# Performance work log

Hardware: AMD Instinct MI355X
Metric: run time of the kernel (lower is better)

Reference implementation:

```python
import jax, jax.numpy as jnp
import numpy as np

B, S, H = 2, 2048, 2048
NH, NKV, HD = 16, 4, 128
LAT = H // 8  # compression_ratio=8


def _rope_tables():
    inv_freq = 1.0 / (10000.0 ** (jnp.arange(0, HD, 2, dtype=jnp.float32) / HD))
    pos = jnp.arange(S, dtype=jnp.float32)
    freqs = pos[:, None] * inv_freq[None, :]          # [S, HD/2]
    emb = jnp.concatenate([freqs, freqs], axis=-1)    # [S, HD]
    return jnp.cos(emb)[None, None], jnp.sin(emb)[None, None]  # [1,1,S,HD]


def setup_inputs() -> dict:
    key = jax.random.key(0)
    ks = jax.random.split(key, 8)
    std = 0.02
    hidden_states = jax.random.normal(ks[0], (B, S, H), dtype=jnp.float32)
    cos, sin = _rope_tables()
    # additive causal mask, broadcast over batch/heads
    causal = jnp.tril(jnp.ones((S, S), dtype=bool))
    attention_mask = jnp.where(causal, 0.0, -1e9).astype(jnp.float32)[None, None]
    Wq = jax.random.normal(ks[1], (H, H), dtype=jnp.float32) * std
    Wk = jax.random.normal(ks[2], (NKV * HD, H), dtype=jnp.float32) * std
    Wv = jax.random.normal(ks[3], (NKV * HD, H), dtype=jnp.float32) * std
    Wo = jax.random.normal(ks[4], (H, H), dtype=jnp.float32) * std
    Wl_in = jax.random.normal(ks[5], (LAT, H), dtype=jnp.float32) * std
    Wl_out = jax.random.normal(ks[6], (H, LAT), dtype=jnp.float32) * std
    latent_gate = jnp.ones((1,), dtype=jnp.float32)
    return dict(hidden_states=hidden_states, cos=cos, sin=sin,
                attention_mask=attention_mask, Wq=Wq, Wk=Wk, Wv=Wv, Wo=Wo,
                Wl_in=Wl_in, Wl_out=Wl_out, latent_gate=latent_gate)


def _rotate_half(x):
    x1, x2 = jnp.split(x, 2, axis=-1)
    return jnp.concatenate([-x2, x1], axis=-1)


def reference(hidden_states, cos, sin, attention_mask, Wq, Wk, Wv, Wo,
              Wl_in, Wl_out, latent_gate):
    b, s, h = hidden_states.shape
    # projections (torch Linear: x @ W.T)
    q = (hidden_states @ Wq.T).reshape(b, s, NH, HD).transpose(0, 2, 1, 3)    # [b,nh,s,hd]
    k = (hidden_states @ Wk.T).reshape(b, s, NKV, HD).transpose(0, 2, 1, 3)   # [b,nkv,s,hd]
    v = (hidden_states @ Wv.T).reshape(b, s, NKV, HD).transpose(0, 2, 1, 3)
    # inline RoPE
    c, sn = cos[:, :, :s, :], sin[:, :, :s, :]
    q = q * c + _rotate_half(q) * sn
    k = k * c + _rotate_half(k) * sn
    # GQA: replicate kv heads (repeat_interleave along head dim)
    rep = NH // NKV
    k = jnp.repeat(k, rep, axis=1)
    v = jnp.repeat(v, rep, axis=1)
    scores = jnp.einsum('bhqd,bhkd->bhqk', q, k) / np.sqrt(HD).astype(np.float32)
    scores = scores + attention_mask
    attn = jax.nn.softmax(scores, axis=-1)
    ctx = jnp.einsum('bhqk,bhkd->bhqd', attn, v)          # [b,nh,s,hd]
    ctx = ctx.transpose(0, 2, 1, 3).reshape(b, s, h)
    attn_out = ctx @ Wo.T
    latent = (hidden_states @ Wl_in.T) @ Wl_out.T          # low-rank residual branch
    return attn_out + latent_gate * latent
```

## Files before the change

### kernel.cpp

```cpp
#include <hip/hip_runtime.h>
#include <hip/hip_bf16.h>

#define Bn   2
#define Sn   2048
#define Hn   2048
#define NHn  16
#define NKVn 4
#define HDn  128
#define LATn 256
#define Mn   (Bn*Sn)
#define KC   2304
#define NWn  3328

typedef unsigned short ushort_t;
typedef __attribute__((ext_vector_type(8))) short bf16x8;
typedef __attribute__((ext_vector_type(8))) unsigned short ushort8;
typedef __attribute__((ext_vector_type(4))) float f32x4;
typedef __attribute__((ext_vector_type(4))) unsigned u32x4;

__device__ __forceinline__ ushort_t f2bf(float f) {
    unsigned u = __float_as_uint(f);
    u += 0x7fffu + ((u >> 16) & 1u);
    return (ushort_t)(u >> 16);
}
__device__ __forceinline__ float bf2f(ushort_t h) {
    return __uint_as_float(((unsigned)h) << 16);
}
__device__ __forceinline__ unsigned cvt_pk_bf16(float lo, float hi) {
    unsigned r;
    asm("v_cvt_pk_bf16_f32 %0, %1, %2" : "=v"(r) : "v"(lo), "v"(hi));
    return r;
}
__device__ __forceinline__ void async16(const void* g, void* l) {
    __builtin_amdgcn_global_load_lds(
        (__attribute__((address_space(1))) void*)g,
        (__attribute__((address_space(3))) void*)l, 16, 0, 0);
}

struct CastArgs {
    const float* src[7];
    ushort_t*    dst[7];
    int n4[7];
    int sshift[7];
    int dcols[7];
    int dcoff[7];
};
__global__ __launch_bounds__(256)
void cast_fused(CastArgs a)
{
    int off = blockIdx.x * 256 + threadIdx.x;
    int seg = 0;
    while (seg < 6 && off >= a.n4[seg]) { off -= a.n4[seg]; ++seg; }
    const int r = off >> a.sshift[seg];
    const int c = off & ((1 << a.sshift[seg]) - 1);
    float4 f = ((const float4*)a.src[seg])[off];
    ushort4 o;
    o.x = f2bf(f.x); o.y = f2bf(f.y); o.z = f2bf(f.z); o.w = f2bf(f.w);
    ((ushort4*)a.dst[seg])[(size_t)r * a.dcols[seg] + a.dcoff[seg] + c] = o;
}

#define GEMM_BK64_LOOP(Aptr, Astr, Wptr, Wstr, Kdim)                          \
    for (int k0 = 0; k0 < (Kdim); k0 += 64) {                                 \
        _Pragma("unroll")                                                     \
        for (int it = 0; it < 4; ++it)                                        \
            async16((Aptr) + (size_t)(m0 + it*32 + srow)*(Astr) + k0 + scol,  \
                    As + (it*256 + tid)*8);                                   \
        _Pragma("unroll")                                                     \
        for (int it = 0; it < 4; ++it)                                        \
            async16((Wptr) + (size_t)(n0 + it*32 + srow)*(Wstr) + k0 + scol,  \
                    Bsm + (it*256 + tid)*8);                                  \
        __syncthreads();                                                      \
        _Pragma("unroll")                                                     \
        for (int hf = 0; hf < 2; ++hf) {                                      \
            bf16x8 af[4], bfr[4];                                             \
            _Pragma("unroll")                                                 \
            for (int mi = 0; mi < 4; ++mi)                                    \
                af[mi] = *(const bf16x8*)(As + aoff[hf*4 + mi]);              \
            _Pragma("unroll")                                                 \
            for (int ni = 0; ni < 4; ++ni)                                    \
                bfr[ni] = *(const bf16x8*)(Bsm + boff[hf*4 + ni]);            \
            _Pragma("unroll")                                                 \
            for (int mi = 0; mi < 4; ++mi)                                    \
                _Pragma("unroll")                                             \
                for (int ni = 0; ni < 4; ++ni)                                \
                    acc[mi][ni] = __builtin_amdgcn_mfma_f32_16x16x32_bf16(    \
                        af[mi], bfr[ni], acc[mi][ni], 0, 0, 0);               \
        }                                                                     \
        __syncthreads();                                                      \
    }

#define GEMM_COMMON_DECLS                                                     \
    const int tid  = threadIdx.x;                                             \
    const int lane = tid & 63, w = tid >> 6;                                  \
    const int t = lane & 15, q = lane >> 4;                                   \
    const int wm = w & 1, wn = w >> 1;                                        \
    const int srow = tid >> 3;                                                \
    const int scol = ((tid & 7) ^ ((tid >> 3) & 7)) * 8;                      \
    int aoff[8], boff[8];                                                     \
    _Pragma("unroll")                                                         \
    for (int hf = 0; hf < 2; ++hf)                                            \
        _Pragma("unroll")                                                     \
        for (int i = 0; i < 4; ++i) {                                         \
            aoff[hf*4 + i] = (wm*64 + i*16 + t)*64 + (((hf*4 + q) ^ (t & 7)) << 3); \
            boff[hf*4 + i] = (wn*64 + i*16 + t)*64 + (((hf*4 + q) ^ (t & 7)) << 3); \
        }                                                                     \
    f32x4 acc[4][4];                                                          \
    _Pragma("unroll")                                                         \
    for (int i = 0; i < 4; ++i)                                               \
        _Pragma("unroll")                                                     \
        for (int j = 0; j < 4; ++j) acc[i][j] = (f32x4){0.f, 0.f, 0.f, 0.f};

__global__ __launch_bounds__(256, 4)
void gemm_qkv(const ushort_t* __restrict__ A, const ushort_t* __restrict__ W,
              ushort_t* __restrict__ qo, ushort_t* __restrict__ ko,
              ushort_t* __restrict__ vo, ushort_t* __restrict__ ctxb,
              const float* __restrict__ gatep,
              const float* __restrict__ cosb, const float* __restrict__ sinb)
{
    __shared__ __align__(16) ushort_t smem[16384];
    ushort_t* As  = smem;
    ushort_t* Bsm = smem + 8192;

    const int m0 = blockIdx.y * 128, n0 = blockIdx.x * 128;
    GEMM_COMMON_DECLS
    GEMM_BK64_LOOP(A, Hn, W, Hn, Hn)

    const int bidx = m0 >> 11, s0 = m0 & (Sn - 1);

    if (n0 >= 2560 && n0 < 3072) {
        const int head = (n0 - 2560) >> 7;
        ushort_t* T = smem;
        #pragma unroll
        for (int h2 = 0; h2 < 2; ++h2) {
            __syncthreads();
            if (wn == h2) {
                #pragma unroll
                for (int mi = 0; mi < 4; ++mi)
                    #pragma unroll
                    for (int ni = 0; ni < 4; ++ni)
                        #pragma unroll
                        for (int r = 0; r < 4; ++r)
                            T[(wm*64 + mi*16 + q*4 + r)*64 + ni*16 + t] =
                                f2bf(acc[mi][ni][r]);
            }
            __syncthreads();
            const int dl = tid >> 2, tseg = (tid & 3) * 32;
            const size_t base =
                ((size_t)(bidx*NKVn + head)*HDn + h2*64 + dl) * Sn + s0 + tseg;
            #pragma unroll
            for (int j0 = 0; j0 < 4; ++j0) {
                ushort8 pk;
                #pragma unroll
                for (int u = 0; u < 8; ++u) {
                    const int p  = j0*8 + u;
                    const int qg = (p >> 3) & 3, j = p & 7;
                    const int orig = (j < 4) ? qg*4 + j : 16 + qg*4 + (j - 4);
                    pk[u] = T[(tseg + orig)*64 + dl];
                }
                *(ushort8*)(vo + base + j0*8) = pk;
            }
        }
        return;
    }

    if (n0 >= 3072) {
        const float gate = gatep[0];
        ushort_t* obase = ctxb + (size_t)m0 * KC + (2048 + (n0 - 3072));
        #pragma unroll
        for (int mi = 0; mi < 4; ++mi)
            #pragma unroll
            for (int r = 0; r < 4; ++r) {
                const int sl = wm*64 + mi*16 + q*4 + r;
                #pragma unroll
                for (int ni = 0; ni < 4; ++ni) {
                    const int d = wn*64 + ni*16 + t;
                    obase[(size_t)sl*KC + d] = f2bf(gate * acc[mi][ni][r]);
                }
            }
        return;
    }

    ushort_t* obase;
    if (n0 < 2048)
        obase = qo + (((size_t)(bidx*NHn + (n0 >> 7)))*Sn + s0) * HDn;
    else
        obase = ko + (((size_t)(bidx*NKVn + ((n0 - 2048) >> 7)))*Sn + s0) * HDn;

    float* smf = (float*)smem;
    if (wn == 1) {
        #pragma unroll
        for (int mi = 0; mi < 4; ++mi)
            #pragma unroll
            for (int r = 0; r < 4; ++r) {
                const int sl = wm*64 + mi*16 + q*4 + r;
                #pragma unroll
                for (int ni = 0; ni < 4; ++ni)
                    smf[sl*64 + (((ni*16 + t) ^ (((sl >> 2) & 3) << 4)))] =
                        acc[mi][ni][r];
            }
    }
    __syncthreads();
    if (wn == 0) {
        #pragma unroll
        for (int mi = 0; mi < 4; ++mi)
            #pragma unroll
            for (int r = 0; r < 4; ++r) {
                const int sl = wm*64 + mi*16 + q*4 + r;
                const int s  = s0 + sl;
                #pragma unroll
                for (int ni = 0; ni < 4; ++ni) {
                    const int d = ni*16 + t;
                    const float c  = cosb[s*HDn + d];
                    const float sn = sinb[s*HDn + d];
                    const float x0 = acc[mi][ni][r];
                    const float x1 = smf[sl*64 + (d ^ (((sl >> 2) & 3) << 4))];
                    obase[(size_t)sl*HDn + d] = f2bf(x0*c - x1*sn);
                }
            }
    }
    __syncthreads();
    if (wn == 0) {
        #pragma unroll
        for (int mi = 0; mi < 4; ++mi)
            #pragma unroll
            for (int r = 0; r < 4; ++r) {
                const int sl = wm*64 + mi*16 + q*4 + r;
                #pragma unroll
                for (int ni = 0; ni < 4; ++ni)
                    smf[sl*64 + (((ni*16 + t) ^ (((sl >> 2) & 3) << 4)))] =
                        acc[mi][ni][r];
            }
    }
    __syncthreads();
    if (wn == 1) {
        #pragma unroll
        for (int mi = 0; mi < 4; ++mi)
            #pragma unroll
            for (int r = 0; r < 4; ++r) {
                const int sl = wm*64 + mi*16 + q*4 + r;
                const int s  = s0 + sl;
                #pragma unroll
                for (int ni = 0; ni < 4; ++ni) {
                    const int dl = ni*16 + t;
                    const int d  = 64 + dl;
                    const float c  = cosb[s*HDn + d];
                    const float sn = sinb[s*HDn + d];
                    const float x1 = acc[mi][ni][r];
                    const float x0 = smf[sl*64 + (dl ^ (((sl >> 2) & 3) << 4))];
                    obase[(size_t)sl*HDn + d] = f2bf(x1*c + x0*sn);
                }
            }
    }
}

__global__ __launch_bounds__(256, 4)
void gemm_out(const ushort_t* __restrict__ A, const ushort_t* __restrict__ W,
              float* __restrict__ outf)
{
    __shared__ __align__(16) ushort_t smem[16384];
    ushort_t* As  = smem;
    ushort_t* Bsm = smem + 8192;

    const int m0 = blockIdx.y * 128, n0 = blockIdx.x * 128;
    GEMM_COMMON_DECLS
    GEMM_BK64_LOOP(A, KC, W, KC, KC)

    #pragma unroll
    for (int mi = 0; mi < 4; ++mi)
        #pragma unroll
        for (int r = 0; r < 4; ++r) {
            const int m = m0 + wm*64 + mi*16 + q*4 + r;
            #pragma unroll
            for (int ni = 0; ni < 4; ++ni) {
                const int n = n0 + wn*64 + ni*16 + t;
                outf[(size_t)m * Hn + n] = acc[mi][ni][r];
            }
        }
}

__global__ __launch_bounds__(256)
void attn_mfma(const ushort_t* __restrict__ qg, const ushort_t* __restrict__ kg,
               const ushort_t* __restrict__ vtg, ushort_t* __restrict__ ctxb)
{
    __shared__ __align__(16) ushort_t Ks[2][8192];
    __shared__ __align__(16) ushort_t Vt[2][8192];

    const int tid = threadIdx.x;
    const int w = tid >> 6, lane = tid & 63;
    const int t = lane & 15, q = lane >> 4;
    const int bh = blockIdx.y;
    const int b = bh >> 4, h = bh & 15;
    const int kvh = h >> 2;
    const ushort_t* qhead  = qg  + ((size_t)(b*NHn  + h  ))*Sn*HDn;
    const ushort_t* khead  = kg  + ((size_t)(b*NKVn + kvh))*Sn*HDn;
    const ushort_t* vthead = vtg + ((size_t)(b*NKVn + kvh))*HDn*Sn;

    const int ksr = tid >> 4;
    const int ksb = (tid & 15) ^ (ksr & 15);
    const int vtr = tid >> 3;
    const int vtb = (tid & 7) ^ (vtr & 7);

    int bko[16], vto[16];
    #pragma unroll
    for (int nb = 0; nb < 4; ++nb)
        #pragma unroll
        for (int ks = 0; ks < 4; ++ks)
            bko[nb*4 + ks] = (nb*16 + t)*128 + (((ks*4 + q) ^ t) << 3);
    #pragma unroll
    for (int d2 = 0; d2 < 8; ++d2)
        #pragma unroll
        for (int ksp = 0; ksp < 2; ++ksp)
            vto[d2*2 + ksp] = (d2*16 + t)*64 + (((ksp*4 + q) ^ (t & 7)) << 3);

    const float cexp2 = 0.12751744737492532f;

    for (int rep = 0; rep < 2; ++rep) {
        const int qt = rep ? (31 - (int)blockIdx.x) : (int)blockIdx.x;

        bf16x8 aq[4];
        #pragma unroll
        for (int ks = 0; ks < 4; ++ks)
            aq[ks] = *(const bf16x8*)(
                qhead + (size_t)(qt*64 + w*16 + t)*HDn + ks*32 + q*8);

        __syncthreads();
        #pragma unroll
        for (int it = 0; it < 4; ++it)
            async16(khead + (size_t)(it*16 + ksr)*HDn + ksb*8,
                    Ks[0] + it*2048 + tid*8);
        #pragma unroll
        for (int it = 0; it < 4; ++it)
            async16(vthead + (size_t)(it*32 + vtr)*Sn + vtb*8,
                    Vt[0] + it*2048 + tid*8);
        __syncthreads();

        float l_sum = 0.f;
        f32x4 O[8];
        #pragma unroll
        for (int d2 = 0; d2 < 8; ++d2) O[d2] = (f32x4){0.f, 0.f, 0.f, 0.f};

        for (int kt = 0; kt <= qt; ++kt) {
            const ushort_t* Kc = Ks[kt & 1];
            const ushort_t* Vc = Vt[kt & 1];

            if (kt < qt) {
                #pragma unroll
                for (int it = 0; it < 4; ++it)
                    async16(khead + (size_t)((kt+1)*64 + it*16 + ksr)*HDn + ksb*8,
                            Ks[(kt & 1) ^ 1] + it*2048 + tid*8);
                #pragma unroll
                for (int it = 0; it < 4; ++it)
                    async16(vthead + (size_t)(it*32 + vtr)*Sn + (kt+1)*64 + vtb*8,
                            Vt[(kt & 1) ^ 1] + it*2048 + tid*8);
            }

            f32x4 sc[4];
            #pragma unroll
            for (int nb = 0; nb < 4; ++nb) {
                sc[nb] = (f32x4){0.f, 0.f, 0.f, 0.f};
                #pragma unroll
                for (int ks = 0; ks < 4; ++ks) {
                    bf16x8 bk = *(const bf16x8*)(Kc + bko[nb*4 + ks]);
                    sc[nb] = __builtin_amdgcn_mfma_f32_16x16x32_bf16(
                        bk, aq[ks], sc[nb], 0, 0, 0);
                }
            }

            float ps[4][4];
            if (kt == qt) {
                const int qi = w*16 + t;
                #pragma unroll
                for (int nb = 0; nb < 4; ++nb)
                    #pragma unroll
                    for (int r = 0; r < 4; ++r) {
                        const int kj = nb*16 + q*4 + r;
                        ps[nb][r] = (kj <= qi) ? exp2f(sc[nb][r]*cexp2) : 0.f;
                    }
            } else {
                #pragma unroll
                for (int nb = 0; nb < 4; ++nb)
                    #pragma unroll
                    for (int r = 0; r < 4; ++r)
                        ps[nb][r] = exp2f(sc[nb][r]*cexp2);
            }
            #pragma unroll
            for (int nb = 0; nb < 4; ++nb)
                #pragma unroll
                for (int r = 0; r < 4; ++r)
                    l_sum += ps[nb][r];

            u32x4 pw0, pw1;
            pw0[0] = cvt_pk_bf16(ps[0][0], ps[0][1]);
            pw0[1] = cvt_pk_bf16(ps[0][2], ps[0][3]);
            pw0[2] = cvt_pk_bf16(ps[1][0], ps[1][1]);
            pw0[3] = cvt_pk_bf16(ps[1][2], ps[1][3]);
            pw1[0] = cvt_pk_bf16(ps[2][0], ps[2][1]);
            pw1[1] = cvt_pk_bf16(ps[2][2], ps[2][3]);
            pw1[2] = cvt_pk_bf16(ps[3][0], ps[3][1]);
            pw1[3] = cvt_pk_bf16(ps[3][2], ps[3][3]);
            const bf16x8 pa0 = __builtin_bit_cast(bf16x8, pw0);
            const bf16x8 pa1 = __builtin_bit_cast(bf16x8, pw1);

            #pragma unroll
            for (int d2 = 0; d2 < 8; ++d2) {
                bf16x8 bv0 = *(const bf16x8*)(Vc + vto[d2*2 + 0]);
                O[d2] = __builtin_amdgcn_mfma_f32_16x16x32_bf16(pa0, bv0, O[d2], 0, 0, 0);
                bf16x8 bv1 = *(const bf16x8*)(Vc + vto[d2*2 + 1]);
                O[d2] = __builtin_amdgcn_mfma_f32_16x16x32_bf16(pa1, bv1, O[d2], 0, 0, 0);
            }

            __syncthreads();
        }

        float lr = l_sum;
        lr += __shfl_xor(lr, 16);
        lr += __shfl_xor(lr, 32);
        float linv[4];
        #pragma unroll
        for (int r = 0; r < 4; ++r)
            linv[r] = 1.f / __shfl(lr, q*4 + r, 16);

        #pragma unroll
        for (int d2 = 0; d2 < 8; ++d2)
            #pragma unroll
            for (int r = 0; r < 4; ++r) {
                const size_t addr =
                    ((size_t)(b*Sn + qt*64 + w*16 + q*4 + r))*KC + h*HDn + d2*16 + t;
                ctxb[addr] = f2bf(O[d2][r] * linv[r]);
            }
    }
}

extern "C" void kernel_launch(void* const* d_in, const int* in_sizes, int n_in,
                              void* d_out, int out_size, void* d_ws, size_t ws_size,
                              hipStream_t stream)
{
    const float* hs    = (const float*)d_in[0];
    const float* cosb  = (const float*)d_in[1];
    const float* sinb  = (const float*)d_in[2];
    const float* Wq    = (const float*)d_in[4];
    const float* Wk    = (const float*)d_in[5];
    const float* Wv    = (const float*)d_in[6];
    const float* Wo    = (const float*)d_in[7];
    const float* Wlin  = (const float*)d_in[8];
    const float* Wlout = (const float*)d_in[9];
    const float* gate  = (const float*)d_in[10];
    float* out = (float*)d_out;

    ushort_t* p = (ushort_t*)d_ws;
    ushort_t* hsb    = p;  p += 8388608;
    ushort_t* Wqkvb  = p;  p += (size_t)NWn*2048;
    ushort_t* Wcomb  = p;  p += 2048*KC;
    ushort_t* qbb    = p;  p += 8388608;
    ushort_t* kbb    = p;  p += 2097152;
    ushort_t* vtb    = p;  p += 2097152;
    ushort_t* ctxc   = p;  p += (size_t)Mn*KC;

    const dim3 blk(256);

    {
        CastArgs ca;
        ca.src[0]=hs;    ca.dst[0]=hsb;                 ca.n4[0]=2097152; ca.sshift[0]=21; ca.dcols[0]=1<<21; ca.dcoff[0]=0;
        ca.src[1]=Wq;    ca.dst[1]=Wqkvb;               ca.n4[1]=1048576; ca.sshift[1]=20; ca.dcols[1]=1<<20; ca.dcoff[1]=0;
        ca.src[2]=Wk;    ca.dst[2]=Wqkvb + 2048*2048;   ca.n4[2]=262144;  ca.sshift[2]=18; ca.dcols[2]=1<<18; ca.dcoff[2]=0;
        ca.src[3]=Wv;    ca.dst[3]=Wqkvb + 2560*2048;   ca.n4[3]=262144;  ca.sshift[3]=18; ca.dcols[3]=1<<18; ca.dcoff[3]=0;
        ca.src[4]=Wlin;  ca.dst[4]=Wqkvb + 3072*2048;   ca.n4[4]=131072;  ca.sshift[4]=17; ca.dcols[4]=1<<17; ca.dcoff[4]=0;
        ca.src[5]=Wo;    ca.dst[5]=Wcomb;               ca.n4[5]=1048576; ca.sshift[5]=9;  ca.dcols[5]=576;   ca.dcoff[5]=0;
        ca.src[6]=Wlout; ca.dst[6]=Wcomb;               ca.n4[6]=131072;  ca.sshift[6]=6;  ca.dcols[6]=576;   ca.dcoff[6]=512;
        cast_fused<<<19456, blk, 0, stream>>>(ca);
    }

    gemm_qkv<<<dim3(26, 32), blk, 0, stream>>>(hsb, Wqkvb, qbb, kbb, vtb, ctxc,
                                               gate, cosb, sinb);

    attn_mfma<<<dim3(16, Bn*NHn), blk, 0, stream>>>(qbb, kbb, vtb, ctxc);

    gemm_out<<<dim3(16, 32), blk, 0, stream>>>(ctxc, Wcomb, out);
}
```

Measured before the change: 313.4 us.

## Fold softmax scale into Q at projection, add MFMA setprio, tree-sum row sums

Moves the softmax scale times log2(e) into the Q projection epilogue, applied after RoPE before the bf16 store. This removes one multiply per score element from the attention inner loop. It also wraps the QK and PV MFMA blocks in s_setprio to raise wave priority during matrix work, and replaces the serial l_sum accumulation with a tree reduction to shorten the dependency chain. Pre-scaling Q before bf16 rounding changes rounding slightly.

```diff
diff --git a/kernel.cpp b/kernel.cpp
--- a/kernel.cpp
+++ b/kernel.cpp
@@ -181,10 +181,14 @@
     }
 
     ushort_t* obase;
-    if (n0 < 2048)
+    float qsc;
+    if (n0 < 2048) {
         obase = qo + (((size_t)(bidx*NHn + (n0 >> 7)))*Sn + s0) * HDn;
-    else
+        qsc = 0.12751744737492532f;
+    } else {
         obase = ko + (((size_t)(bidx*NKVn + ((n0 - 2048) >> 7)))*Sn + s0) * HDn;
+        qsc = 1.0f;
+    }
 
     float* smf = (float*)smem;
     if (wn == 1) {
@@ -214,7 +218,7 @@
                     const float sn = sinb[s*HDn + d];
                     const float x0 = acc[mi][ni][r];
                     const float x1 = smf[sl*64 + (d ^ (((sl >> 2) & 3) << 4))];
-                    obase[(size_t)sl*HDn + d] = f2bf(x0*c - x1*sn);
+                    obase[(size_t)sl*HDn + d] = f2bf(qsc*(x0*c - x1*sn));
                 }
             }
     }
@@ -247,7 +251,7 @@
                     const float sn = sinb[s*HDn + d];
                     const float x1 = acc[mi][ni][r];
                     const float x0 = smf[sl*64 + (dl ^ (((sl >> 2) & 3) << 4))];
-                    obase[(size_t)sl*HDn + d] = f2bf(x1*c + x0*sn);
+                    obase[(size_t)sl*HDn + d] = f2bf(qsc*(x1*c + x0*sn));
                 }
             }
     }
@@ -312,8 +316,6 @@
         for (int ksp = 0; ksp < 2; ++ksp)
             vto[d2*2 + ksp] = (d2*16 + t)*64 + (((ksp*4 + q) ^ (t & 7)) << 3);
 
-    const float cexp2 = 0.12751744737492532f;
-
     for (int rep = 0; rep < 2; ++rep) {
         const int qt = rep ? (31 - (int)blockIdx.x) : (int)blockIdx.x;
 
@@ -355,6 +357,7 @@
             }
 
             f32x4 sc[4];
+            __builtin_amdgcn_s_setprio(1);
             #pragma unroll
             for (int nb = 0; nb < 4; ++nb) {
                 sc[nb] = (f32x4){0.f, 0.f, 0.f, 0.f};
@@ -365,6 +368,7 @@
                         bk, aq[ks], sc[nb], 0, 0, 0);
                 }
             }
+            __builtin_amdgcn_s_setprio(0);
 
             float ps[4][4];
             if (kt == qt) {
@@ -374,20 +378,22 @@
                     #pragma unroll
                     for (int r = 0; r < 4; ++r) {
                         const int kj = nb*16 + q*4 + r;
-                        ps[nb][r] = (kj <= qi) ? exp2f(sc[nb][r]*cexp2) : 0.f;
+                        ps[nb][r] = (kj <= qi) ? exp2f(sc[nb][r]) : 0.f;
                     }
             } else {
                 #pragma unroll
                 for (int nb = 0; nb < 4; ++nb)
                     #pragma unroll
                     for (int r = 0; r < 4; ++r)
-                        ps[nb][r] = exp2f(sc[nb][r]*cexp2);
-            }
-            #pragma unroll
-            for (int nb = 0; nb < 4; ++nb)
-                #pragma unroll
-                for (int r = 0; r < 4; ++r)
-                    l_sum += ps[nb][r];
+                        ps[nb][r] = exp2f(sc[nb][r]);
+            }
+            {
+                float t0 = (ps[0][0] + ps[0][1]) + (ps[0][2] + ps[0][3]);
+                float t1 = (ps[1][0] + ps[1][1]) + (ps[1][2] + ps[1][3]);
+                float t2 = (ps[2][0] + ps[2][1]) + (ps[2][2] + ps[2][3]);
+                float t3 = (ps[3][0] + ps[3][1]) + (ps[3][2] + ps[3][3]);
+                l_sum += (t0 + t1) + (t2 + t3);
+            }
 
             u32x4 pw0, pw1;
             pw0[0] = cvt_pk_bf16(ps[0][0], ps[0][1]);
@@ -401,6 +407,7 @@
             const bf16x8 pa0 = __builtin_bit_cast(bf16x8, pw0);
             const bf16x8 pa1 = __builtin_bit_cast(bf16x8, pw1);
 
+            __builtin_amdgcn_s_setprio(1);
             #pragma unroll
             for (int d2 = 0; d2 < 8; ++d2) {
                 bf16x8 bv0 = *(const bf16x8*)(Vc + vto[d2*2 + 0]);
@@ -408,6 +415,7 @@
                 bf16x8 bv1 = *(const bf16x8*)(Vc + vto[d2*2 + 1]);
                 O[d2] = __builtin_amdgcn_mfma_f32_16x16x32_bf16(pa1, bv1, O[d2], 0, 0, 0);
             }
+            __builtin_amdgcn_s_setprio(0);
 
             __syncthreads();
         }
```

After: 319.9 us, median of 2. 1.02x slower.
